# Kernel optimization log

Hardware: AMD Instinct MI355X
Metric: run time of the kernel (lower is better)

The kernel has to match this reference:

```python
import jax, jax.numpy as jnp
import numpy as np

B, C, H, W = 16, 256, 64, 64
HEADS = 4  # kvl produces (heads-1)=3 groups: lfeat, k, v


def setup_inputs() -> dict:
    key = jax.random.key(0)
    ks = jax.random.split(key, 8)
    s = 0.02
    return {
        "x": jax.random.normal(ks[0], (B, C, H, W), jnp.float32),
        "q_input": jax.random.normal(ks[1], (B, C, H, W), jnp.float32),
        "w_kvl": jax.random.normal(ks[2], (C * (HEADS - 1), C), jnp.float32) * s,
        "b_kvl": jnp.zeros((C * (HEADS - 1),), jnp.float32),
        "w_q": jax.random.normal(ks[3], (C, C), jnp.float32) * s,
        "b_q": jnp.zeros((C,), jnp.float32),
        "w_proj": jax.random.normal(ks[4], (C, 2 * C), jnp.float32) * s,
        "b_proj": jnp.zeros((C,), jnp.float32),
    }


def gelu(x):
    return jax.nn.gelu(x, approximate=False)  # torch nn.GELU default (erf)


def reference(x, q_input, w_kvl, b_kvl, w_q, b_q, w_proj, b_proj):
    b, c, h, w = x.shape
    n = h * w
    # 1x1 conv kvl: C -> 3C, then GELU
    kvl = gelu(jnp.einsum('oc,bchw->bohw', w_kvl, x) + b_kvl[None, :, None, None])
    kvl = kvl.reshape(b, HEADS - 1, c, h, w)
    lfeat = kvl[:, 0]                      # [B,C,H,W]
    k = kvl[:, 1].reshape(b, c, n)          # [B,C,HW]
    v = kvl[:, 2].reshape(b, c, n)          # [B,C,HW]
    # 1x1 conv q: C -> C
    q = jnp.einsum('oc,bchw->bohw', w_q, q_input) + b_q[None, :, None, None]
    q = q.reshape(b, c, n)                  # [B,C,HW]
    # channel-wise attention: qk is [B,C,C] (no scaling, per source)
    qk = jnp.einsum('bcn,bdn->bcd', q, k)
    qk = jax.nn.softmax(qk, axis=-1)
    x2 = jnp.einsum('bcd,bdn->bcn', qk, v).reshape(b, c, h, w)
    cat = jnp.concatenate([lfeat, x2], axis=1)  # [B,2C,H,W]
    out = jnp.einsum('oc,bchw->bohw', w_proj, cat) + b_proj[None, :, None, None]
    return gelu(out)
```

## Files before the change

### kernel.cpp

```cpp
#include <hip/hip_runtime.h>
#include <hip/hip_bf16.h>
#include <hip/hip_fp16.h>

typedef _Float16 f16;
typedef _Float16 half8 __attribute__((ext_vector_type(8)));
typedef float f32x4 __attribute__((ext_vector_type(4)));

#define BM 128
#define BN 128
#define BK 32

__device__ __forceinline__ float gelu_f(float x) {
  return 0.5f * x * (1.0f + erff(x * 0.70710678118654752f));
}

__device__ __forceinline__ void gll16(const void* g, void* l) {
  __builtin_amdgcn_global_load_lds((const __attribute__((address_space(1))) void*)g,
                                   (__attribute__((address_space(3))) void*)l,
                                   16, 0, 0);
}

template<int BIAS, bool GELU_ACT, bool OUT_F16, bool KSPLIT>
__global__ __launch_bounds__(256)
void gemm_tn(const f16* __restrict__ P, size_t sP, int ldP,
             const f16* __restrict__ Q, size_t sQ, int ldQ,
             void* __restrict__ Dv, size_t sD, int ldD,
             const float* __restrict__ bias,
             int M, int N, int K, int nks)
{
  __shared__ __align__(16) f16 ldsA[BM * BK];
  __shared__ __align__(16) f16 ldsB[BM * BK];

  const int t = threadIdx.x;
  const int l = t & 63;
  const int wid = t >> 6;
  const int wr = wid >> 1;
  const int wc = wid & 1;

  const int z = blockIdx.z;
  const int b = z / nks;
  const int s = z - b * nks;
  const int kLen = K / nks;
  const int k0 = s * kLen;

  const int mBase = blockIdx.y * BM;
  const int nBase = blockIdx.x * BN;

  const f16* Pb = P + (size_t)b * sP;
  const f16* Qb = Q + (size_t)b * sQ;

  f32x4 acc[4][4];
#pragma unroll
  for (int i = 0; i < 4; ++i)
#pragma unroll
    for (int j = 0; j < 4; ++j)
      acc[i][j] = (f32x4){0.f, 0.f, 0.f, 0.f};

  const int nk = kLen / BK;
  for (int kt = 0; kt < nk; ++kt) {
    const int kk = k0 + kt * BK;
#pragma unroll
    for (int c = 0; c < 2; ++c) {
      const int off = c * 4096 + wid * 1024 + l * 16;
      const int row = off >> 6;
      const int gch = ((off >> 4) & 3) ^ ((row >> 1) & 3);
      gll16(Pb + (size_t)(mBase + row) * ldP + kk + gch * 8,
            (char*)ldsA + c * 4096 + wid * 1024);
      gll16(Qb + (size_t)(nBase + row) * ldQ + kk + gch * 8,
            (char*)ldsB + c * 4096 + wid * 1024);
    }
    asm volatile("s_waitcnt vmcnt(0)" ::: "memory");
    __syncthreads();

    half8 af[4], bf[4];
#pragma unroll
    for (int mi = 0; mi < 4; ++mi) {
      const int row = wr * 64 + mi * 16 + (l & 15);
      const int phys = row * 64 + ((((l >> 4) ^ (row >> 1)) & 3) << 4);
      af[mi] = *(const half8*)((const char*)ldsA + phys);
    }
#pragma unroll
    for (int ni = 0; ni < 4; ++ni) {
      const int row = wc * 64 + ni * 16 + (l & 15);
      const int phys = row * 64 + ((((l >> 4) ^ (row >> 1)) & 3) << 4);
      bf[ni] = *(const half8*)((const char*)ldsB + phys);
    }
#pragma unroll
    for (int mi = 0; mi < 4; ++mi)
#pragma unroll
      for (int ni = 0; ni < 4; ++ni)
        acc[mi][ni] = __builtin_amdgcn_mfma_f32_16x16x32_f16(af[mi], bf[ni], acc[mi][ni], 0, 0, 0);
    __syncthreads();
  }

  float* Dsplit = nullptr; f16* D16 = nullptr; float* D32 = nullptr;
  if (KSPLIT)      Dsplit = (float*)Dv + (size_t)z * (size_t)(M * N);
  else if (OUT_F16) D16   = (f16*)Dv + (size_t)b * sD;
  else              D32   = (float*)Dv + (size_t)b * sD;

#pragma unroll
  for (int mi = 0; mi < 4; ++mi) {
    const int rb = mBase + wr * 64 + mi * 16 + ((l >> 4) << 2);
#pragma unroll
    for (int ni = 0; ni < 4; ++ni) {
      const int col = nBase + wc * 64 + ni * 16 + (l & 15);
#pragma unroll
      for (int j = 0; j < 4; ++j) {
        float v = acc[mi][ni][j];
        const int rr = rb + j;
        if (BIAS == 1) v += bias[rr];
        if (BIAS == 2) v += bias[col];
        if (GELU_ACT) v = gelu_f(v);
        if (KSPLIT)       Dsplit[(size_t)rr * ldD + col] = v;
        else if (OUT_F16) D16[(size_t)rr * ldD + col] = (f16)v;
        else              D32[(size_t)rr * ldD + col] = v;
      }
    }
  }
}

__global__ __launch_bounds__(256)
void transpose_cvt(const float* __restrict__ in, f16* __restrict__ outp) {
  __shared__ float tile[32][33];
  const int b = blockIdx.z;
  const int c0 = blockIdx.y * 32;
  const int n0 = blockIdx.x * 32;
  const int tx = threadIdx.x & 31;
  const int ty = threadIdx.x >> 5;
  const float* ib = in + (size_t)b * (256 * 4096);
  f16* ob = outp + (size_t)b * (256 * 4096);
#pragma unroll
  for (int i = 0; i < 4; ++i)
    tile[ty + i * 8][tx] = ib[(size_t)(c0 + ty + i * 8) * 4096 + n0 + tx];
  __syncthreads();
#pragma unroll
  for (int i = 0; i < 4; ++i)
    ob[(size_t)(n0 + ty + i * 8) * 256 + c0 + tx] = (f16)tile[tx][ty + i * 8];
}

__global__ void cvt16(const float* __restrict__ in, f16* __restrict__ outp, int n) {
  int i = blockIdx.x * blockDim.x + threadIdx.x;
  if (i < n) outp[i] = (f16)in[i];
}

__global__ __launch_bounds__(256)
void softmax_k(const float* __restrict__ qkp, f16* __restrict__ p, int nks) {
  const int t = threadIdx.x;
  const int wid = t >> 6, l = t & 63;
  const int r = blockIdx.x * 4 + wid;
  const int b = r >> 8, c = r & 255;
  float v[4] = {0.f, 0.f, 0.f, 0.f};
  for (int s = 0; s < nks; ++s) {
    const float* base = qkp + (size_t)(b * nks + s) * 65536 + (size_t)c * 256;
#pragma unroll
    for (int j = 0; j < 4; ++j) v[j] += base[l + 64 * j];
  }
  float m = fmaxf(fmaxf(v[0], v[1]), fmaxf(v[2], v[3]));
#pragma unroll
  for (int off = 32; off; off >>= 1) m = fmaxf(m, __shfl_xor(m, off));
  float e[4], sum = 0.f;
#pragma unroll
  for (int j = 0; j < 4; ++j) { e[j] = expf(v[j] - m); sum += e[j]; }
#pragma unroll
  for (int off = 32; off; off >>= 1) sum += __shfl_xor(sum, off);
  const float inv = 1.0f / sum;
  f16* pb = p + (size_t)r * 256;
#pragma unroll
  for (int j = 0; j < 4; ++j) pb[l + 64 * j] = (f16)(e[j] * inv);
}

extern "C" void kernel_launch(void* const* d_in, const int* in_sizes, int n_in,
                              void* d_out, int out_size, void* d_ws, size_t ws_size,
                              hipStream_t stream) {
  const float* x      = (const float*)d_in[0];
  const float* qin    = (const float*)d_in[1];
  const float* w_kvl  = (const float*)d_in[2];
  const float* b_kvl  = (const float*)d_in[3];
  const float* w_q    = (const float*)d_in[4];
  const float* b_q    = (const float*)d_in[5];
  const float* w_proj = (const float*)d_in[6];
  const float* b_proj = (const float*)d_in[7];
  float* out = (float*)d_out;
  char* ws = (char*)d_ws;

  if (ws_size < 235667456) return;

  f16* xt   = (f16*)(ws + 0);
  f16* qt   = (f16*)(ws + 33554432);
  f16* wk   = (f16*)(ws + 67108864);
  f16* wq   = (f16*)(ws + 67502080);
  f16* wp   = (f16*)(ws + 67633152);
  f16* kH   = (f16*)(ws + 67895296);
  f16* qH   = (f16*)(ws + 101449728);
  f16* vt   = (f16*)(ws + 135004160);
  f16* catT = (f16*)(ws + 168558592);
  float* qkp = (float*)xt;
  f16* pH = qt;

  const size_t sAct = 1048576;
  dim3 blk(256);

  transpose_cvt<<<dim3(128, 8, 16), blk, 0, stream>>>(x, xt);
  transpose_cvt<<<dim3(128, 8, 16), blk, 0, stream>>>(qin, qt);
  cvt16<<<dim3(768), blk, 0, stream>>>(w_kvl, wk, 196608);
  cvt16<<<dim3(256), blk, 0, stream>>>(w_q, wq, 65536);
  cvt16<<<dim3(512), blk, 0, stream>>>(w_proj, wp, 131072);

  hipLaunchKernelGGL((gemm_tn<1, true, true, false>), dim3(32, 2, 16), blk, 0, stream,
      wk + 65536, (size_t)0, 256, xt, sAct, 256,
      (void*)kH, sAct, 4096, b_kvl + 256, 256, 4096, 256, 1);
  hipLaunchKernelGGL((gemm_tn<2, true, true, false>), dim3(2, 32, 16), blk, 0, stream,
      xt, sAct, 256, wk, (size_t)0, 256,
      (void*)catT, (size_t)2097152, 512, b_kvl, 4096, 256, 256, 1);
  hipLaunchKernelGGL((gemm_tn<2, true, true, false>), dim3(2, 32, 16), blk, 0, stream,
      xt, sAct, 256, wk + 131072, (size_t)0, 256,
      (void*)vt, sAct, 256, b_kvl + 512, 4096, 256, 256, 1);
  hipLaunchKernelGGL((gemm_tn<1, false, true, false>), dim3(32, 2, 16), blk, 0, stream,
      wq, (size_t)0, 256, qt, sAct, 256,
      (void*)qH, sAct, 4096, b_q, 256, 4096, 256, 1);
  hipLaunchKernelGGL((gemm_tn<0, false, false, true>), dim3(2, 2, 128), blk, 0, stream,
      qH, sAct, 4096, kH, sAct, 4096,
      (void*)qkp, (size_t)0, 256, (const float*)nullptr, 256, 256, 4096, 8);
  softmax_k<<<dim3(1024), blk, 0, stream>>>(qkp, pH, 8);
  hipLaunchKernelGGL((gemm_tn<0, false, true, false>), dim3(2, 32, 16), blk, 0, stream,
      vt, sAct, 256, pH, (size_t)65536, 256,
      (void*)(catT + 256), (size_t)2097152, 512, (const float*)nullptr, 4096, 256, 256, 1);
  hipLaunchKernelGGL((gemm_tn<1, true, false, false>), dim3(32, 2, 16), blk, 0, stream,
      wp, (size_t)0, 512, catT, (size_t)2097152, 512,
      (void*)out, sAct, 4096, b_proj, 256, 4096, 512, 1);
}
```

Baseline: 432.3 us.

## Reassociate q projection into qk product and double-buffer GEMM LDS

Rewrites qk = (Wq·Qin + bq)·K^T as Wq·(Qin·K^T) + bq·rowsum(K). The large q projection GEMM and the transpose of q_input go away, and a small 256x256 GEMM per batch plus a K row-sum kernel take their place. The GEMM mainloop now double-buffers LDS so global loads overlap the MFMA work, and the weight conversion kernels use vectorized half8 stores. The reassociation changes rounding order, since the Qin·K^T partials are reduced and rounded to fp16 before the Wq multiply, which may affect accuracy.

```diff
diff --git a/kernel.cpp b/kernel.cpp
--- a/kernel.cpp
+++ b/kernel.cpp
@@ -4,6 +4,7 @@
 
 typedef _Float16 f16;
 typedef _Float16 half8 __attribute__((ext_vector_type(8)));
+typedef _Float16 half4 __attribute__((ext_vector_type(4)));
 typedef float f32x4 __attribute__((ext_vector_type(4)));
 
 #define BM 128
@@ -25,11 +26,10 @@
 void gemm_tn(const f16* __restrict__ P, size_t sP, int ldP,
              const f16* __restrict__ Q, size_t sQ, int ldQ,
              void* __restrict__ Dv, size_t sD, int ldD,
-             const float* __restrict__ bias,
+             const float* __restrict__ bias, const float* __restrict__ bias2,
              int M, int N, int K, int nks)
 {
-  __shared__ __align__(16) f16 ldsA[BM * BK];
-  __shared__ __align__(16) f16 ldsB[BM * BK];
+  __shared__ __align__(16) char lds[32768];
 
   const int t = threadIdx.x;
   const int l = t & 63;
@@ -49,6 +49,19 @@
   const f16* Pb = P + (size_t)b * sP;
   const f16* Qb = Q + (size_t)b * sQ;
 
+  const f16* srcA[2];
+  const f16* srcB[2];
+  int dstOff[2];
+#pragma unroll
+  for (int c = 0; c < 2; ++c) {
+    const int off = c * 4096 + wid * 1024 + l * 16;
+    const int row = off >> 6;
+    const int gch = ((off >> 4) & 3) ^ ((row >> 1) & 3);
+    srcA[c] = Pb + (size_t)(mBase + row) * ldP + k0 + gch * 8;
+    srcB[c] = Qb + (size_t)(nBase + row) * ldQ + k0 + gch * 8;
+    dstOff[c] = c * 4096 + wid * 1024;
+  }
+
   f32x4 acc[4][4];
 #pragma unroll
   for (int i = 0; i < 4; ++i)
@@ -56,47 +69,53 @@
     for (int j = 0; j < 4; ++j)
       acc[i][j] = (f32x4){0.f, 0.f, 0.f, 0.f};
 
-  const int nk = kLen / BK;
-  for (int kt = 0; kt < nk; ++kt) {
-    const int kk = k0 + kt * BK;
+  auto stage = [&](int buf) {
 #pragma unroll
     for (int c = 0; c < 2; ++c) {
-      const int off = c * 4096 + wid * 1024 + l * 16;
-      const int row = off >> 6;
-      const int gch = ((off >> 4) & 3) ^ ((row >> 1) & 3);
-      gll16(Pb + (size_t)(mBase + row) * ldP + kk + gch * 8,
-            (char*)ldsA + c * 4096 + wid * 1024);
-      gll16(Qb + (size_t)(nBase + row) * ldQ + kk + gch * 8,
-            (char*)ldsB + c * 4096 + wid * 1024);
-    }
-    asm volatile("s_waitcnt vmcnt(0)" ::: "memory");
-    __syncthreads();
-
+      gll16(srcA[c], lds + buf * 8192 + dstOff[c]);
+      gll16(srcB[c], lds + 16384 + buf * 8192 + dstOff[c]);
+      srcA[c] += BK;
+      srcB[c] += BK;
+    }
+  };
+
+  auto compute = [&](int buf) {
     half8 af[4], bf[4];
 #pragma unroll
     for (int mi = 0; mi < 4; ++mi) {
       const int row = wr * 64 + mi * 16 + (l & 15);
       const int phys = row * 64 + ((((l >> 4) ^ (row >> 1)) & 3) << 4);
-      af[mi] = *(const half8*)((const char*)ldsA + phys);
+      af[mi] = *(const half8*)(lds + buf * 8192 + phys);
     }
 #pragma unroll
     for (int ni = 0; ni < 4; ++ni) {
       const int row = wc * 64 + ni * 16 + (l & 15);
       const int phys = row * 64 + ((((l >> 4) ^ (row >> 1)) & 3) << 4);
-      bf[ni] = *(const half8*)((const char*)ldsB + phys);
+      bf[ni] = *(const half8*)(lds + 16384 + buf * 8192 + phys);
     }
 #pragma unroll
     for (int mi = 0; mi < 4; ++mi)
 #pragma unroll
       for (int ni = 0; ni < 4; ++ni)
         acc[mi][ni] = __builtin_amdgcn_mfma_f32_16x16x32_f16(af[mi], bf[ni], acc[mi][ni], 0, 0, 0);
+  };
+
+  const int nk = kLen / BK;
+  stage(0);
+  __syncthreads();
+  int cur = 0;
+  for (int kt = 0; kt < nk - 1; ++kt) {
+    stage(cur ^ 1);
+    compute(cur);
     __syncthreads();
-  }
+    cur ^= 1;
+  }
+  compute(cur);
 
   float* Dsplit = nullptr; f16* D16 = nullptr; float* D32 = nullptr;
-  if (KSPLIT)      Dsplit = (float*)Dv + (size_t)z * (size_t)(M * N);
-  else if (OUT_F16) D16   = (f16*)Dv + (size_t)b * sD;
-  else              D32   = (float*)Dv + (size_t)b * sD;
+  if (KSPLIT)       Dsplit = (float*)Dv + (size_t)z * (size_t)(M * N);
+  else if (OUT_F16) D16    = (f16*)Dv + (size_t)b * sD;
+  else              D32    = (float*)Dv + (size_t)b * sD;
 
 #pragma unroll
   for (int mi = 0; mi < 4; ++mi) {
@@ -110,6 +129,7 @@
         const int rr = rb + j;
         if (BIAS == 1) v += bias[rr];
         if (BIAS == 2) v += bias[col];
+        if (BIAS == 3) v += bias[rr] * bias2[(size_t)b * N + col];
         if (GELU_ACT) v = gelu_f(v);
         if (KSPLIT)       Dsplit[(size_t)rr * ldD + col] = v;
         else if (OUT_F16) D16[(size_t)rr * ldD + col] = (f16)v;
@@ -138,23 +158,59 @@
     ob[(size_t)(n0 + ty + i * 8) * 256 + c0 + tx] = (f16)tile[tx][ty + i * 8];
 }
 
-__global__ void cvt16(const float* __restrict__ in, f16* __restrict__ outp, int n) {
-  int i = blockIdx.x * blockDim.x + threadIdx.x;
-  if (i < n) outp[i] = (f16)in[i];
-}
-
-__global__ __launch_bounds__(256)
-void softmax_k(const float* __restrict__ qkp, f16* __restrict__ p, int nks) {
-  const int t = threadIdx.x;
-  const int wid = t >> 6, l = t & 63;
-  const int r = blockIdx.x * 4 + wid;
-  const int b = r >> 8, c = r & 255;
-  float v[4] = {0.f, 0.f, 0.f, 0.f};
-  for (int s = 0; s < nks; ++s) {
-    const float* base = qkp + (size_t)(b * nks + s) * 65536 + (size_t)c * 256;
-#pragma unroll
-    for (int j = 0; j < 4; ++j) v[j] += base[l + 64 * j];
-  }
+__global__ __launch_bounds__(256)
+void cvtf16(const float* __restrict__ in, f16* __restrict__ outp, int n8) {
+  int i = blockIdx.x * 256 + threadIdx.x;
+  if (i < n8) {
+    float4 a = ((const float4*)in)[2 * i];
+    float4 c = ((const float4*)in)[2 * i + 1];
+    half8 h = {(f16)a.x, (f16)a.y, (f16)a.z, (f16)a.w,
+               (f16)c.x, (f16)c.y, (f16)c.z, (f16)c.w};
+    ((half8*)outp)[i] = h;
+  }
+}
+
+__global__ __launch_bounds__(256)
+void ksum_k(const f16* __restrict__ kH, float* __restrict__ ks) {
+  const int r = blockIdx.x * 4 + (threadIdx.x >> 6);
+  const int l = threadIdx.x & 63;
+  const half8* row = (const half8*)(kH + (size_t)r * 4096);
+  float s = 0.f;
+#pragma unroll
+  for (int j = 0; j < 8; ++j) {
+    half8 h = row[l + 64 * j];
+#pragma unroll
+    for (int e = 0; e < 8; ++e) s += (float)h[e];
+  }
+#pragma unroll
+  for (int off = 32; off; off >>= 1) s += __shfl_xor(s, off);
+  if (l == 0) ks[r] = s;
+}
+
+__global__ __launch_bounds__(256)
+void reduce8_k(const float* __restrict__ part, f16* __restrict__ m1T) {
+  const int i = blockIdx.x * 256 + threadIdx.x;
+  const int b = i >> 14;
+  const int e4 = i & 16383;
+  const float4* base = (const float4*)part + (size_t)b * 131072 + e4;
+  float4 s = {0.f, 0.f, 0.f, 0.f};
+#pragma unroll
+  for (int zz = 0; zz < 8; ++zz) {
+    float4 p = base[(size_t)zz * 16384];
+    s.x += p.x; s.y += p.y; s.z += p.z; s.w += p.w;
+  }
+  half4 h = {(f16)s.x, (f16)s.y, (f16)s.z, (f16)s.w};
+  ((half4*)m1T)[i] = h;
+}
+
+__global__ __launch_bounds__(256)
+void softmax_row(const float* __restrict__ qk, f16* __restrict__ p) {
+  const int r = blockIdx.x * 4 + (threadIdx.x >> 6);
+  const int l = threadIdx.x & 63;
+  const float* row = qk + (size_t)r * 256;
+  float v[4];
+#pragma unroll
+  for (int j = 0; j < 4; ++j) v[j] = row[l + 64 * j];
   float m = fmaxf(fmaxf(v[0], v[1]), fmaxf(v[2], v[3]));
 #pragma unroll
   for (int off = 32; off; off >>= 1) m = fmaxf(m, __shfl_xor(m, off));
@@ -183,49 +239,58 @@
   float* out = (float*)d_out;
   char* ws = (char*)d_ws;
 
-  if (ws_size < 235667456) return;
-
-  f16* xt   = (f16*)(ws + 0);
-  f16* qt   = (f16*)(ws + 33554432);
-  f16* wk   = (f16*)(ws + 67108864);
-  f16* wq   = (f16*)(ws + 67502080);
-  f16* wp   = (f16*)(ws + 67633152);
-  f16* kH   = (f16*)(ws + 67895296);
-  f16* qH   = (f16*)(ws + 101449728);
-  f16* vt   = (f16*)(ws + 135004160);
-  f16* catT = (f16*)(ws + 168558592);
-  float* qkp = (float*)xt;
-  f16* pH = qt;
+  if (ws_size < 202129408) return;
+
+  f16*   xt    = (f16*)(ws + 0);
+  float* part  = (float*)(ws + 0);
+  f16*   qin16 = (f16*)(ws + 33554432);
+  f16*   m1T   = (f16*)(ws + 33554432);
+  float* qkb   = (float*)(ws + 35651584);
+  f16*   pH    = (f16*)(ws + 39845888);
+  f16*   wk16  = (f16*)(ws + 67108864);
+  f16*   wq16  = (f16*)(ws + 67502080);
+  f16*   wp16  = (f16*)(ws + 67633152);
+  float* ksum  = (float*)(ws + 67895296);
+  f16*   kH    = (f16*)(ws + 67911680);
+  f16*   vt    = (f16*)(ws + 101466112);
+  f16*   catT  = (f16*)(ws + 135020544);
 
   const size_t sAct = 1048576;
   dim3 blk(256);
 
   transpose_cvt<<<dim3(128, 8, 16), blk, 0, stream>>>(x, xt);
-  transpose_cvt<<<dim3(128, 8, 16), blk, 0, stream>>>(qin, qt);
-  cvt16<<<dim3(768), blk, 0, stream>>>(w_kvl, wk, 196608);
-  cvt16<<<dim3(256), blk, 0, stream>>>(w_q, wq, 65536);
-  cvt16<<<dim3(512), blk, 0, stream>>>(w_proj, wp, 131072);
+  cvtf16<<<dim3(8192), blk, 0, stream>>>(qin, qin16, 2097152);
+  cvtf16<<<dim3(96),  blk, 0, stream>>>(w_kvl, wk16, 24576);
+  cvtf16<<<dim3(32),  blk, 0, stream>>>(w_q, wq16, 8192);
+  cvtf16<<<dim3(64),  blk, 0, stream>>>(w_proj, wp16, 16384);
 
   hipLaunchKernelGGL((gemm_tn<1, true, true, false>), dim3(32, 2, 16), blk, 0, stream,
-      wk + 65536, (size_t)0, 256, xt, sAct, 256,
-      (void*)kH, sAct, 4096, b_kvl + 256, 256, 4096, 256, 1);
+      wk16 + 65536, (size_t)0, 256, xt, sAct, 256,
+      (void*)kH, sAct, 4096, b_kvl + 256, (const float*)nullptr, 256, 4096, 256, 1);
   hipLaunchKernelGGL((gemm_tn<2, true, true, false>), dim3(2, 32, 16), blk, 0, stream,
-      xt, sAct, 256, wk, (size_t)0, 256,
-      (void*)catT, (size_t)2097152, 512, b_kvl, 4096, 256, 256, 1);
+      xt, sAct, 256, wk16, (size_t)0, 256,
+      (void*)catT, (size_t)2097152, 512, b_kvl, (const float*)nullptr, 4096, 256, 256, 1);
   hipLaunchKernelGGL((gemm_tn<2, true, true, false>), dim3(2, 32, 16), blk, 0, stream,
-      xt, sAct, 256, wk + 131072, (size_t)0, 256,
-      (void*)vt, sAct, 256, b_kvl + 512, 4096, 256, 256, 1);
-  hipLaunchKernelGGL((gemm_tn<1, false, true, false>), dim3(32, 2, 16), blk, 0, stream,
-      wq, (size_t)0, 256, qt, sAct, 256,
-      (void*)qH, sAct, 4096, b_q, 256, 4096, 256, 1);
+      xt, sAct, 256, wk16 + 131072, (size_t)0, 256,
+      (void*)vt, sAct, 256, b_kvl + 512, (const float*)nullptr, 4096, 256, 256, 1);
+
+  ksum_k<<<dim3(1024), blk, 0, stream>>>(kH, ksum);
+
   hipLaunchKernelGGL((gemm_tn<0, false, false, true>), dim3(2, 2, 128), blk, 0, stream,
-      qH, sAct, 4096, kH, sAct, 4096,
-      (void*)qkp, (size_t)0, 256, (const float*)nullptr, 256, 256, 4096, 8);
-  softmax_k<<<dim3(1024), blk, 0, stream>>>(qkp, pH, 8);
+      kH, sAct, 4096, qin16, sAct, 4096,
+      (void*)part, (size_t)0, 256, (const float*)nullptr, (const float*)nullptr, 256, 256, 4096, 8);
+  reduce8_k<<<dim3(1024), blk, 0, stream>>>(part, m1T);
+
+  hipLaunchKernelGGL((gemm_tn<3, false, false, false>), dim3(2, 2, 16), blk, 0, stream,
+      wq16, (size_t)0, 256, m1T, (size_t)65536, 256,
+      (void*)qkb, (size_t)65536, 256, b_q, ksum, 256, 256, 256, 1);
+
+  softmax_row<<<dim3(1024), blk, 0, stream>>>(qkb, pH);
+
   hipLaunchKernelGGL((gemm_tn<0, false, true, false>), dim3(2, 32, 16), blk, 0, stream,
       vt, sAct, 256, pH, (size_t)65536, 256,
-      (void*)(catT + 256), (size_t)2097152, 512, (const float*)nullptr, 4096, 256, 256, 1);
+      (void*)(catT + 256), (size_t)2097152, 512, (const float*)nullptr, (const float*)nullptr, 4096, 256, 256, 1);
   hipLaunchKernelGGL((gemm_tn<1, true, false, false>), dim3(32, 2, 16), blk, 0, stream,
-      wp, (size_t)0, 512, catT, (size_t)2097152, 512,
-      (void*)out, sAct, 4096, b_proj, 256, 4096, 512, 1);
-}
+      wp16, (size_t)0, 512, catT, (size_t)2097152, 512,
+      (void*)out, sAct, 4096, b_proj, (const float*)nullptr, 256, 4096, 512, 1);
+}
```

Result: slower. 488.4 us (+13.0%).
